# Optimization experiments

Measured on AMD Instinct MI355X. Metric: run time of the kernel, lower is better.

Reference implementation:

```python
import jax, jax.numpy as jnp
import numpy as np

HID = 1024; INTER = 2048; NSTATE = 16; KCONV = 4; DTRANK = 64
NHEADS = 16; NKV = 4; HDIM = 64; VHDIM = 128; EPS = 1e-6
ATTN_H = HID; K_H = NKV * HDIM; V_H = NKV * VHDIM
LATENT = INTER + ATTN_H + K_H + V_H  # 3840


def rmsnorm(x, w, eps=EPS):
    return x * jax.lax.rsqrt(jnp.mean(x * x, axis=-1, keepdims=True) + eps) * w


def setup_inputs():
    key = jax.random.key(0)
    ks = jax.random.split(key, 8)
    B, S = 2, 2048
    s = 0.02
    x = jax.random.normal(ks[0], (B, S, HID), jnp.float32)
    W_in = jax.random.normal(ks[1], (LATENT + INTER, HID), jnp.float32) * s
    conv_w = jax.random.normal(ks[2], (INTER, KCONV), jnp.float32) * 0.2
    conv_b = jnp.zeros((INTER,), jnp.float32)
    W_x = jax.random.normal(ks[3], (DTRANK + 2 * NSTATE, INTER), jnp.float32) * s
    dt_ln_w = jnp.ones((DTRANK,), jnp.float32)
    B_ln_w = jnp.ones((NSTATE,), jnp.float32)
    C_ln_w = jnp.ones((NSTATE,), jnp.float32)
    W_dt = jax.random.normal(ks[4], (INTER, DTRANK), jnp.float32) * s
    b_dt = jnp.log(jnp.expm1(jnp.full((INTER,), 0.01, jnp.float32)))
    A_log = jnp.log(jnp.broadcast_to(jnp.arange(1, NSTATE + 1, dtype=jnp.float32)[None, :], (INTER, NSTATE)))
    D_param = jnp.ones((INTER,), jnp.float32)
    ln1_w = jnp.ones((INTER,), jnp.float32)
    ln2_w = jnp.ones((INTER,), jnp.float32)
    W_out = jax.random.normal(ks[5], (HID, INTER), jnp.float32) * s
    return {"x": x, "W_in": W_in, "conv_w": conv_w, "conv_b": conv_b, "W_x": W_x,
            "dt_ln_w": dt_ln_w, "B_ln_w": B_ln_w, "C_ln_w": C_ln_w, "W_dt": W_dt,
            "b_dt": b_dt, "A_log": A_log, "D_param": D_param, "ln1_w": ln1_w,
            "ln2_w": ln2_w, "W_out": W_out}


def reference(x, W_in, conv_w, conv_b, W_x, dt_ln_w, B_ln_w, C_ln_w, W_dt, b_dt,
              A_log, D_param, ln1_w, ln2_w, W_out):
    Bsz, S, _ = x.shape
    proj = x @ W_in.T  # [B,S,LATENT+INTER]
    q = proj[..., :ATTN_H]
    k = proj[..., ATTN_H:ATTN_H + K_H]
    v = proj[..., ATTN_H + K_H:ATTN_H + K_H + V_H]
    xs = proj[..., ATTN_H + K_H + V_H:LATENT]
    gate = proj[..., LATENT:]

    # depthwise causal conv1d + silu (causal_conv1d_fn)
    xt = xs.transpose(0, 2, 1)  # [B,D,S]
    xc = jax.lax.conv_general_dilated(xt, conv_w[:, None, :], (1,), [(KCONV - 1, 0)],
                                      feature_group_count=INTER,
                                      dimension_numbers=("NCH", "OIH", "NCH"))
    xc = jax.nn.silu(xc + conv_b[None, :, None]).transpose(0, 2, 1)  # [B,S,D]

    # input-dependent dt, B, C with inner RMSNorms
    ssm_p = xc @ W_x.T  # [B,S,DTRANK+2N]
    dt = rmsnorm(ssm_p[..., :DTRANK], dt_ln_w)
    Bm = rmsnorm(ssm_p[..., DTRANK:DTRANK + NSTATE], B_ln_w)
    Cm = rmsnorm(ssm_p[..., DTRANK + NSTATE:], C_ln_w)
    delta = jax.nn.softplus(dt @ W_dt.T + b_dt)  # [B,S,D] (delta_bias + softplus)
    A = -jnp.exp(A_log)  # [D,N]

    def step(h, inp):
        d_t, b_t, c_t, x_t = inp  # [B,D],[B,N],[B,N],[B,D]
        dA = jnp.exp(d_t[:, :, None] * A)  # [B,D,N]
        h = h * dA + (d_t * x_t)[:, :, None] * b_t[:, None, :]
        y = jnp.einsum("bdn,bn->bd", h, c_t)
        return h, y

    h0 = jnp.zeros((Bsz, INTER, NSTATE), x.dtype)
    _, ys = jax.lax.scan(step, h0, (delta.transpose(1, 0, 2), Bm.transpose(1, 0, 2),
                                    Cm.transpose(1, 0, 2), xc.transpose(1, 0, 2)))
    y = ys.transpose(1, 0, 2) + xc * D_param
    y = y * jax.nn.silu(gate)  # gated scan output [B,S,INTER]

    # causal GQA attention branch (no output proj; v_head_dim = INTER/NHEADS)
    qh = q.reshape(Bsz, S, NHEADS, HDIM).transpose(0, 2, 1, 3)
    kh = jnp.repeat(k.reshape(Bsz, S, NKV, HDIM), NHEADS // NKV, axis=2).transpose(0, 2, 1, 3)
    vh = jnp.repeat(v.reshape(Bsz, S, NKV, VHDIM), NHEADS // NKV, axis=2).transpose(0, 2, 1, 3)
    scores = jnp.einsum("bhqd,bhkd->bhqk", qh, kh) * (1.0 / float(np.sqrt(HDIM)))
    mask = jnp.tril(jnp.ones((S, S), bool))
    scores = jnp.where(mask, scores, jnp.finfo(scores.dtype).min)
    attn = jnp.einsum("bhqk,bhkd->bhqd", jax.nn.softmax(scores, axis=-1), vh)
    attn = attn.transpose(0, 2, 1, 3).reshape(Bsz, S, INTER)

    out = (rmsnorm(attn, ln1_w) + rmsnorm(y, ln2_w)) * 0.5
    return out @ W_out.T
```

## Files before the change

### kernel.cpp

```cpp
#include <hip/hip_runtime.h>
#include <stdint.h>

#define HID    1024
#define INTER  2048
#define NSTATE 16
#define DTRANK 64
#define NHEADS 16
#define NKV    4
#define HDIM   64
#define VHDIM  128
#define ATTN_H 1024
#define K_H    256
#define V_H    512
#define LATENT 3840
#define NCOLS  5888
#define BATCH  2
#define SEQ    2048
#define T_TOT  4096
#define NCHUNK 64
#define CHLEN  32

typedef __bf16 bf16x8 __attribute__((ext_vector_type(8)));
typedef float  f32x4  __attribute__((ext_vector_type(4)));
typedef float  f32x4v __attribute__((ext_vector_type(4)));
typedef unsigned short u16x8 __attribute__((ext_vector_type(8)));

__device__ __forceinline__ float bf2f(unsigned short u) {
    return __uint_as_float(((unsigned int)u) << 16);
}
__device__ __forceinline__ unsigned short f2bf(float f) {
    unsigned int u = __float_as_uint(f);
    u = (u + 0x7fffu + ((u >> 16) & 1u)) >> 16;
    return (unsigned short)u;
}
__device__ __forceinline__ bf16x8 ldb8(const unsigned short* p) {
    return __builtin_bit_cast(bf16x8, *(const u16x8*)p);
}

typedef const __attribute__((address_space(1))) unsigned int* gas_ptr;
typedef __attribute__((address_space(3))) unsigned int* las_ptr;
__device__ __forceinline__ void load_lds16(const void* g, void* l) {
    __builtin_amdgcn_global_load_lds((gas_ptr)g, (las_ptr)l, 16, 0, 0);
}

__global__ void k_cvt(const float* __restrict__ src, unsigned short* __restrict__ dst, int n8) {
    int i = blockIdx.x * blockDim.x + threadIdx.x;
    if (i >= n8) return;
    f32x4v a = ((const f32x4v*)src)[2 * i];
    f32x4v b = ((const f32x4v*)src)[2 * i + 1];
    u16x8 o;
#pragma unroll
    for (int k = 0; k < 4; k++) { o[k] = f2bf(a[k]); o[k + 4] = f2bf(b[k]); }
    *(u16x8*)(dst + (size_t)i * 8) = o;
}

__global__ void k_wxpad(const float* __restrict__ W_x, unsigned short* __restrict__ Wxpad) {
    int i = blockIdx.x * blockDim.x + threadIdx.x;
    int e = i * 8;
    int row = e >> 11;
    int col = e & 2047;
    u16x8 o;
    if (row < DTRANK + 2 * NSTATE) {
#pragma unroll
        for (int k = 0; k < 8; k++) o[k] = f2bf(W_x[(size_t)row * INTER + col + k]);
    } else {
#pragma unroll
        for (int k = 0; k < 8; k++) o[k] = 0;
    }
    *(u16x8*)(Wxpad + e) = o;
}

template <int OUT_MODE>
__launch_bounds__(256)
__global__ void k_gemm(const unsigned short* __restrict__ A, const unsigned short* __restrict__ B,
                       void* __restrict__ Cout, const float* __restrict__ bias,
                       int M, int N, int K, int lda, int ldb, int ldc) {
    __shared__ __align__(16) unsigned short As[128 * 64];
    __shared__ __align__(16) unsigned short Bs[128 * 64];
    const int tid = threadIdx.x;
    const int lane = tid & 63;
    const int w = tid >> 6;
    const int wm = w >> 1, wn = w & 1;
    const int bm = blockIdx.y * 128, bn = blockIdx.x * 128;
    const size_t koff = (OUT_MODE == 3) ? (size_t)blockIdx.z * K : 0;

    f32x4 acc[4][4];
#pragma unroll
    for (int i = 0; i < 4; i++)
#pragma unroll
        for (int j = 0; j < 4; j++) acc[i][j] = (f32x4){0.f, 0.f, 0.f, 0.f};

    const int nk = K >> 6;
    for (int ks = 0; ks < nk; ++ks) {
        const int k0 = ks << 6;
#pragma unroll
        for (int i = 0; i < 4; ++i) {
            int qb = (w << 6) + (i << 8);
            int q = qb + lane;
            int row = q >> 3, c = q & 7;
            int csrc = c ^ (row & 7);
            load_lds16(A + (size_t)(bm + row) * lda + koff + k0 + csrc * 8, As + qb * 8);
            load_lds16(B + (size_t)(bn + row) * ldb + koff + k0 + csrc * 8, Bs + qb * 8);
        }
        __syncthreads();
#pragma unroll
        for (int kk = 0; kk < 2; ++kk) {
            bf16x8 af[4], bfr[4];
#pragma unroll
            for (int mi = 0; mi < 4; mi++) {
                int row = (wm << 6) + (mi << 4) + (lane & 15);
                int c = (kk << 2) + (lane >> 4);
                af[mi] = ldb8(As + row * 64 + (c ^ (row & 7)) * 8);
            }
#pragma unroll
            for (int ni = 0; ni < 4; ni++) {
                int row = (wn << 6) + (ni << 4) + (lane & 15);
                int c = (kk << 2) + (lane >> 4);
                bfr[ni] = ldb8(Bs + row * 64 + (c ^ (row & 7)) * 8);
            }
#pragma unroll
            for (int mi = 0; mi < 4; mi++)
#pragma unroll
                for (int ni = 0; ni < 4; ni++)
                    acc[mi][ni] = __builtin_amdgcn_mfma_f32_16x16x32_bf16(af[mi], bfr[ni], acc[mi][ni], 0, 0, 0);
        }
        __syncthreads();
    }
#pragma unroll
    for (int mi = 0; mi < 4; mi++)
#pragma unroll
        for (int ni = 0; ni < 4; ni++)
#pragma unroll
            for (int r = 0; r < 4; r++) {
                int grow = bm + (wm << 6) + (mi << 4) + ((lane >> 4) << 2) + r;
                int gcol = bn + (wn << 6) + (ni << 4) + (lane & 15);
                float v = acc[mi][ni][r];
                if (OUT_MODE == 0) {
                    ((unsigned short*)Cout)[(size_t)grow * ldc + gcol] = f2bf(v);
                } else if (OUT_MODE == 1) {
                    ((float*)Cout)[(size_t)grow * ldc + gcol] = v;
                } else if (OUT_MODE == 3) {
                    ((float*)Cout)[(size_t)blockIdx.z * M * ldc + (size_t)grow * ldc + gcol] = v;
                } else {
                    v += bias[gcol];
                    v = (v > 20.f) ? v : log1pf(__expf(v));
                    ((unsigned short*)Cout)[(size_t)grow * ldc + gcol] = f2bf(v);
                }
            }
}

__global__ void k_conv(const unsigned short* __restrict__ proj, const float* __restrict__ conv_w,
                       const float* __restrict__ conv_b, unsigned short* __restrict__ xc) {
    int r = blockIdx.x;
    int d8 = threadIdx.x * 8;
    int t = r & (SEQ - 1);
    float accv[8];
#pragma unroll
    for (int i = 0; i < 8; i++) accv[i] = conv_b[d8 + i];
#pragma unroll
    for (int j = 0; j < 4; j++) {
        int tp = t - 3 + j;
        if (tp < 0) continue;
        u16x8 xv = *(const u16x8*)(proj + (size_t)(r - 3 + j) * NCOLS + (LATENT - INTER) + d8);
#pragma unroll
        for (int i = 0; i < 8; i++) accv[i] += conv_w[(d8 + i) * 4 + j] * bf2f(xv[i]);
    }
    u16x8 o;
#pragma unroll
    for (int i = 0; i < 8; i++) {
        float v = accv[i];
        v = v / (1.f + __expf(-v));
        o[i] = f2bf(v);
    }
    *(u16x8*)(xc + (size_t)r * INTER + d8) = o;
}

__global__ void k_rms3(const float* __restrict__ ssmp, const float* __restrict__ dt_w,
                       const float* __restrict__ B_w, const float* __restrict__ C_w,
                       unsigned short* __restrict__ dtbf, float* __restrict__ Bm, float* __restrict__ Cm) {
    int r = blockIdx.x;
    int tid = threadIdx.x;
    int lane = tid & 63, w = tid >> 6;
    int c = tid;
    float v = 0.f;
    if (c < 96) {
#pragma unroll
        for (int s = 0; s < 8; s++) v += ssmp[(size_t)s * (T_TOT * 128) + (size_t)r * 128 + c];
    }
    float s = v * v;
    if (w == 0) {
#pragma unroll
        for (int d = 1; d < 64; d <<= 1) s += __shfl_xor(s, d);
        float rms = rsqrtf(s * (1.f / 64.f) + 1e-6f);
        dtbf[(size_t)r * 64 + lane] = f2bf(v * rms * dt_w[lane]);
    } else {
#pragma unroll
        for (int d = 1; d < 16; d <<= 1) s += __shfl_xor(s, d);
        float rms = rsqrtf(s * (1.f / 16.f) + 1e-6f);
        if (lane < 16) Bm[(size_t)r * 16 + lane] = v * rms * B_w[lane];
        else if (lane < 32) Cm[(size_t)r * 16 + (lane - 16)] = v * rms * C_w[lane - 16];
    }
}

template <int PASS>
__launch_bounds__(256)
__global__ void k_scan_chunk(const unsigned short* __restrict__ deltabf, const unsigned short* __restrict__ xcbf,
                             const float* __restrict__ Bm, const float* __restrict__ Cm,
                             const float* __restrict__ A_log,
                             float* __restrict__ hend, float* __restrict__ sumd,
                             const float* __restrict__ hinit, unsigned short* __restrict__ ybf) {
    __shared__ __align__(16) unsigned short dltS[CHLEN * 256];
    __shared__ __align__(16) unsigned short xvS[CHLEN * 256];
    __shared__ __align__(16) float BsT[CHLEN * 16];
    __shared__ __align__(16) float CsT[CHLEN * 16];
    const int d0 = blockIdx.x * 256;
    const int c = blockIdx.y;
    const int b = blockIdx.z;
    const int tid = threadIdx.x, lane = tid & 63, w = tid >> 6;
    const int t0 = c * CHLEN;
    const size_t rowbase = (size_t)(b * SEQ + t0);

    float An[16];
    {
        const f32x4* ap = (const f32x4*)(A_log + (size_t)(d0 + tid) * 16);
#pragma unroll
        for (int n4 = 0; n4 < 4; n4++) {
            f32x4 av = ap[n4];
#pragma unroll
            for (int j = 0; j < 4; j++) An[n4 * 4 + j] = -__expf(av[j]);
        }
    }

#pragma unroll
    for (int i = 0; i < 4; ++i) {
        int qb = (w << 6) + (i << 8);
        int q = qb + lane;
        int t = q >> 5, coff = q & 31;
        load_lds16(deltabf + (rowbase + t) * INTER + d0 + coff * 8, dltS + qb * 8);
        load_lds16(xcbf + (rowbase + t) * INTER + d0 + coff * 8, xvS + qb * 8);
    }
    if (tid < 128) {
        ((f32x4*)BsT)[tid] = ((const f32x4*)(Bm + rowbase * 16))[tid];
        if (PASS == 2) ((f32x4*)CsT)[tid] = ((const f32x4*)(Cm + rowbase * 16))[tid];
    }
    __syncthreads();

    const size_t sidx = ((size_t)(c * BATCH + b) * INTER + d0 + tid) * 16;
    float h[16];
    if (PASS == 2) {
        const f32x4* hp = (const f32x4*)(hinit + sidx);
#pragma unroll
        for (int n4 = 0; n4 < 4; n4++) {
            f32x4 hv = hp[n4];
#pragma unroll
            for (int j = 0; j < 4; j++) h[n4 * 4 + j] = hv[j];
        }
    } else {
#pragma unroll
        for (int n = 0; n < 16; n++) h[n] = 0.f;
    }
    float sd = 0.f;
    for (int t = 0; t < CHLEN; ++t) {
        float dlt = bf2f(dltS[t * 256 + tid]);
        float xv = bf2f(xvS[t * 256 + tid]);
        float dx = dlt * xv;
        if (PASS == 0) sd += dlt;
        float y = 0.f;
#pragma unroll
        for (int n4 = 0; n4 < 4; ++n4) {
            f32x4 Bt = ((f32x4*)BsT)[t * 4 + n4];
            f32x4 Ct;
            if (PASS == 2) Ct = ((f32x4*)CsT)[t * 4 + n4];
#pragma unroll
            for (int j = 0; j < 4; ++j) {
                int n = n4 * 4 + j;
                float a = __expf(dlt * An[n]);
                h[n] = h[n] * a + dx * Bt[j];
                if (PASS == 2) y += h[n] * Ct[j];
            }
        }
        if (PASS == 2) ybf[(rowbase + t) * INTER + d0 + tid] = f2bf(y);
    }
    if (PASS == 0) {
        f32x4* hp = (f32x4*)(hend + sidx);
#pragma unroll
        for (int n4 = 0; n4 < 4; n4++) {
            f32x4 hv;
#pragma unroll
            for (int j = 0; j < 4; j++) hv[j] = h[n4 * 4 + j];
            hp[n4] = hv;
        }
        sumd[(size_t)(c * BATCH + b) * INTER + d0 + tid] = sd;
    }
}

__global__ void k_scan_prop(const float* __restrict__ A_log, const float* __restrict__ hend,
                            const float* __restrict__ sumd, float* __restrict__ hinit) {
    const int tid = blockIdx.x * 256 + threadIdx.x;
    const int n = tid & 15;
    const int d = (tid >> 4) & (INTER - 1);
    const float An = -__expf(A_log[(size_t)d * 16 + n]);
    const int bd = tid >> 4;
    float h = 0.f;
#pragma unroll 1
    for (int cb = 0; cb < NCHUNK / 4; ++cb) {
        float he[4], sdv[4];
#pragma unroll
        for (int j = 0; j < 4; j++) {
            int c = cb * 4 + j;
            he[j] = hend[(size_t)c * 65536 + tid];
            sdv[j] = sumd[(size_t)c * 4096 + bd];
        }
#pragma unroll
        for (int j = 0; j < 4; j++) {
            int c = cb * 4 + j;
            hinit[(size_t)c * 65536 + tid] = h;
            h = he[j] + __expf(An * sdv[j]) * h;
        }
    }
}

__launch_bounds__(256)
__global__ void k_attn(const unsigned short* __restrict__ proj, unsigned short* __restrict__ attn) {
    __shared__ __align__(16) unsigned short Ks[64 * 64];
    __shared__ __align__(16) unsigned short Vt[128 * 64];
    __shared__ __align__(16) unsigned short Ps[4 * 16 * 64];
    const int pair = blockIdx.x;
    const int h = blockIdx.y;
    const int b = blockIdx.z;
    const int g = h >> 2;
    const int tid = threadIdx.x, lane = tid & 63, w = tid >> 6;
    const int l15 = lane & 15, hi = lane >> 4;

    const int krow = tid >> 3, kc = tid & 7;
    const int kp2 = (tid & 31) * 2, vb = tid >> 5;

    const unsigned short* kbase = proj + (size_t)(b * SEQ) * NCOLS + ATTN_H + g * HDIM;
    const unsigned short* vbase = proj + (size_t)(b * SEQ) * NCOLS + (ATTN_H + K_H) + g * VHDIM;

    u16x8 krA[2], vrA[2][2], krB[2], vrB[2][2];

    auto LOAD = [&](u16x8* kr, u16x8 (*vr)[2], int kv) {
        const unsigned short* kp_ = kbase + (size_t)(kv + krow) * NCOLS + kc * 8;
        kr[0] = *(const u16x8*)kp_;
        kr[1] = *(const u16x8*)(kp_ + (size_t)32 * NCOLS);
        const unsigned short* vp_ = vbase + (size_t)(kv + kp2) * NCOLS + vb * 8;
        vr[0][0] = *(const u16x8*)vp_;
        vr[0][1] = *(const u16x8*)(vp_ + NCOLS);
        vr[1][0] = *(const u16x8*)(vp_ + 64);
        vr[1][1] = *(const u16x8*)(vp_ + NCOLS + 64);
    };
    auto WRITE = [&](u16x8* kr, u16x8 (*vr)[2]) {
        int ksw = (kc ^ (krow & 7)) << 3;
        *(u16x8*)&Ks[krow * 64 + ksw] = kr[0];
        *(u16x8*)&Ks[(krow + 32) * 64 + ksw] = kr[1];
#pragma unroll
        for (int hf = 0; hf < 2; hf++) {
            u16x8 va = vr[hf][0], vb2 = vr[hf][1];
#pragma unroll
            for (int i = 0; i < 8; i++) {
                unsigned int pk = (unsigned int)va[i] | ((unsigned int)vb2[i] << 16);
                int r = (vb + hf * 8) * 8 + i;
                *(unsigned int*)&Vt[r * 64 + (((kp2 >> 3) ^ (r & 7)) << 3) + (kp2 & 7)] = pk;
            }
        }
    };

    const float SC = 0.18033688f;

    for (int phase = 0; phase < 2; ++phase) {
        const int qt = (phase == 0) ? (31 - pair) : pair;
        const int qw = qt * 64 + w * 16;
        const int ntiles = qt + 1;

        bf16x8 qf[2];
        {
            int qr = qw + l15;
            const unsigned short* qp = proj + (size_t)(b * SEQ + qr) * NCOLS + h * HDIM + hi * 8;
            qf[0] = ldb8(qp);
            qf[1] = ldb8(qp + 32);
        }
        f32x4 O[8];
#pragma unroll
        for (int vf = 0; vf < 8; vf++) O[vf] = (f32x4){0.f, 0.f, 0.f, 0.f};
        float l_[4] = {0.f, 0.f, 0.f, 0.f};

        auto COMPUTE = [&](int kv) {
            const int pbase = w * 1024;
            f32x4 sv[4];
#pragma unroll
            for (int cf = 0; cf < 4; ++cf) {
                f32x4 s = (f32x4){0.f, 0.f, 0.f, 0.f};
                int row = cf * 16 + l15;
#pragma unroll
                for (int kk = 0; kk < 2; ++kk) {
                    bf16x8 kb = ldb8(&Ks[row * 64 + ((((kk << 2) + hi) ^ (row & 7)) << 3)]);
                    s = __builtin_amdgcn_mfma_f32_16x16x32_bf16(qf[kk], kb, s, 0, 0, 0);
                }
                sv[cf] = s;
            }
            const int qi0 = qw + (hi << 2);
#pragma unroll
            for (int cf = 0; cf < 4; ++cf) {
                int ki = kv + cf * 16 + l15;
#pragma unroll
                for (int rg = 0; rg < 4; ++rg) {
                    float v = (ki <= qi0 + rg) ? exp2f(sv[cf][rg] * SC) : 0.f;
                    l_[rg] += v;
                    int pr = (hi << 2) + rg;
                    int pc = cf * 16 + l15;
                    Ps[pbase + pr * 64 + (((pc >> 3) ^ (pr & 7)) << 3) + (pc & 7)] = f2bf(v);
                }
            }
            bf16x8 pa0 = ldb8(&Ps[pbase + l15 * 64 + ((hi ^ (l15 & 7)) << 3)]);
            bf16x8 pa1 = ldb8(&Ps[pbase + l15 * 64 + (((4 + hi) ^ (l15 & 7)) << 3)]);
#pragma unroll
            for (int vf = 0; vf < 8; ++vf) {
                int vr_ = vf * 16 + l15;
                bf16x8 v0 = ldb8(&Vt[vr_ * 64 + ((hi ^ (vr_ & 7)) << 3)]);
                bf16x8 v1 = ldb8(&Vt[vr_ * 64 + (((4 + hi) ^ (vr_ & 7)) << 3)]);
                O[vf] = __builtin_amdgcn_mfma_f32_16x16x32_bf16(pa0, v0, O[vf], 0, 0, 0);
                O[vf] = __builtin_amdgcn_mfma_f32_16x16x32_bf16(pa1, v1, O[vf], 0, 0, 0);
            }
        };

        LOAD(krA, vrA, 0);
        bool useA = true;
        for (int j = 0; j < ntiles; ++j) {
            if (useA) {
                WRITE(krA, vrA);
                if (j + 1 < ntiles) LOAD(krB, vrB, (j + 1) * 64);
            } else {
                WRITE(krB, vrB);
                if (j + 1 < ntiles) LOAD(krA, vrA, (j + 1) * 64);
            }
            __syncthreads();
            COMPUTE(j * 64);
            __syncthreads();
            useA = !useA;
        }

#pragma unroll
        for (int dd = 1; dd < 16; dd <<= 1)
#pragma unroll
            for (int rg = 0; rg < 4; ++rg) l_[rg] += __shfl_xor(l_[rg], dd);
#pragma unroll
        for (int rg = 0; rg < 4; ++rg) {
            float inv = 1.f / l_[rg];
            int grow = b * SEQ + qw + (hi << 2) + rg;
#pragma unroll
            for (int vf = 0; vf < 8; ++vf) {
                int gcol = h * VHDIM + vf * 16 + l15;
                attn[(size_t)grow * INTER + gcol] = f2bf(O[vf][rg] * inv);
            }
        }
    }
}

__launch_bounds__(256)
__global__ void k_fuse(const unsigned short* __restrict__ attn, const unsigned short* __restrict__ ybf,
                       const unsigned short* __restrict__ xc, const unsigned short* __restrict__ proj,
                       const float* __restrict__ Dp, const float* __restrict__ ln1,
                       const float* __restrict__ ln2, unsigned short* __restrict__ fused) {
    __shared__ float red[8];
    int r = blockIdx.x, tid = threadIdx.x;
    int c8 = tid * 8;
    u16x8 av = *(const u16x8*)(attn + (size_t)r * INTER + c8);
    u16x8 yv8 = *(const u16x8*)(ybf + (size_t)r * INTER + c8);
    u16x8 xv8 = *(const u16x8*)(xc + (size_t)r * INTER + c8);
    u16x8 gv8 = *(const u16x8*)(proj + (size_t)r * NCOLS + LATENT + c8);
    float a_[8], y_[8];
    float ssa = 0.f, ssy = 0.f;
#pragma unroll
    for (int i = 0; i < 8; i++) {
        float a = bf2f(av[i]);
        float yv = bf2f(yv8[i]) + bf2f(xv8[i]) * Dp[c8 + i];
        float gg = bf2f(gv8[i]);
        yv *= gg / (1.f + __expf(-gg));
        a_[i] = a; y_[i] = yv;
        ssa += a * a; ssy += yv * yv;
    }
#pragma unroll
    for (int d = 1; d < 64; d <<= 1) { ssa += __shfl_xor(ssa, d); ssy += __shfl_xor(ssy, d); }
    int w = tid >> 6, lane = tid & 63;
    if (lane == 0) { red[w * 2] = ssa; red[w * 2 + 1] = ssy; }
    __syncthreads();
    ssa = red[0] + red[2] + red[4] + red[6];
    ssy = red[1] + red[3] + red[5] + red[7];
    float ra = rsqrtf(ssa * (1.f / 2048.f) + 1e-6f);
    float ry = rsqrtf(ssy * (1.f / 2048.f) + 1e-6f);
    u16x8 o;
#pragma unroll
    for (int i = 0; i < 8; i++) {
        float v = (a_[i] * ra * ln1[c8 + i] + y_[i] * ry * ln2[c8 + i]) * 0.5f;
        o[i] = f2bf(v);
    }
    *(u16x8*)(fused + (size_t)r * INTER + c8) = o;
}

extern "C" void kernel_launch(void* const* d_in, const int* in_sizes, int n_in,
                              void* d_out, int out_size, void* d_ws, size_t ws_size,
                              hipStream_t stream) {
    const float* x      = (const float*)d_in[0];
    const float* W_in   = (const float*)d_in[1];
    const float* conv_w = (const float*)d_in[2];
    const float* conv_b = (const float*)d_in[3];
    const float* W_x    = (const float*)d_in[4];
    const float* dt_w   = (const float*)d_in[5];
    const float* B_w    = (const float*)d_in[6];
    const float* C_w    = (const float*)d_in[7];
    const float* W_dt   = (const float*)d_in[8];
    const float* b_dt   = (const float*)d_in[9];
    const float* A_log  = (const float*)d_in[10];
    const float* Dp     = (const float*)d_in[11];
    const float* ln1    = (const float*)d_in[12];
    const float* ln2    = (const float*)d_in[13];
    const float* W_out  = (const float*)d_in[14];
    float* out = (float*)d_out;

    char* p = (char*)d_ws;
    auto alloc = [&](size_t bytes) -> void* {
        void* r = (void*)p;
        p += (bytes + 255) & ~(size_t)255;
        return r;
    };
    unsigned short* xbf     = (unsigned short*)alloc((size_t)T_TOT * HID * 2);
    unsigned short* Winbf   = (unsigned short*)alloc((size_t)NCOLS * HID * 2);
    unsigned short* projbf  = (unsigned short*)alloc((size_t)T_TOT * NCOLS * 2);
    unsigned short* xcbf    = (unsigned short*)alloc((size_t)T_TOT * INTER * 2);
    unsigned short* Wxpad   = (unsigned short*)alloc((size_t)128 * INTER * 2);
    float*          ssmp    = (float*)alloc((size_t)8 * T_TOT * 128 * 4);
    unsigned short* dtbf    = (unsigned short*)alloc((size_t)T_TOT * DTRANK * 2);
    float*          Bm      = (float*)alloc((size_t)T_TOT * 16 * 4);
    float*          Cm      = (float*)alloc((size_t)T_TOT * 16 * 4);
    unsigned short* Wdtbf   = (unsigned short*)alloc((size_t)INTER * DTRANK * 2);
    unsigned short* deltabf = (unsigned short*)alloc((size_t)T_TOT * INTER * 2);
    unsigned short* ybf     = (unsigned short*)alloc((size_t)T_TOT * INTER * 2);
    unsigned short* attnbf  = (unsigned short*)alloc((size_t)T_TOT * INTER * 2);
    unsigned short* fusedbf = (unsigned short*)alloc((size_t)T_TOT * INTER * 2);
    unsigned short* Woutbf  = (unsigned short*)alloc((size_t)HID * INTER * 2);
    float*          hendws  = (float*)alloc((size_t)NCHUNK * BATCH * INTER * 16 * 4);
    float*          hinitws = (float*)alloc((size_t)NCHUNK * BATCH * INTER * 16 * 4);
    float*          sumdws  = (float*)alloc((size_t)NCHUNK * BATCH * INTER * 4);

    k_cvt<<<(T_TOT * HID / 8 + 255) / 256, 256, 0, stream>>>(x, xbf, T_TOT * HID / 8);
    k_cvt<<<(NCOLS * HID / 8 + 255) / 256, 256, 0, stream>>>(W_in, Winbf, NCOLS * HID / 8);
    k_cvt<<<(INTER * DTRANK / 8 + 255) / 256, 256, 0, stream>>>(W_dt, Wdtbf, INTER * DTRANK / 8);
    k_cvt<<<(HID * INTER / 8 + 255) / 256, 256, 0, stream>>>(W_out, Woutbf, HID * INTER / 8);
    k_wxpad<<<(128 * INTER / 8) / 256, 256, 0, stream>>>(W_x, Wxpad);

    k_gemm<0><<<dim3(NCOLS / 128, T_TOT / 128), 256, 0, stream>>>(
        xbf, Winbf, projbf, nullptr, T_TOT, NCOLS, HID, HID, HID, NCOLS);
    k_conv<<<T_TOT, 256, 0, stream>>>(projbf, conv_w, conv_b, xcbf);
    k_gemm<3><<<dim3(1, T_TOT / 128, 8), 256, 0, stream>>>(
        xcbf, Wxpad, ssmp, nullptr, T_TOT, 128, 256, INTER, INTER, 128);
    k_rms3<<<T_TOT, 128, 0, stream>>>(ssmp, dt_w, B_w, C_w, dtbf, Bm, Cm);
    k_gemm<2><<<dim3(INTER / 128, T_TOT / 128), 256, 0, stream>>>(
        dtbf, Wdtbf, deltabf, b_dt, T_TOT, INTER, DTRANK, DTRANK, DTRANK, INTER);
    k_scan_chunk<0><<<dim3(INTER / 256, NCHUNK, BATCH), 256, 0, stream>>>(
        deltabf, xcbf, Bm, Cm, A_log, hendws, sumdws, nullptr, nullptr);
    k_scan_prop<<<256, 256, 0, stream>>>(A_log, hendws, sumdws, hinitws);
    k_scan_chunk<2><<<dim3(INTER / 256, NCHUNK, BATCH), 256, 0, stream>>>(
        deltabf, xcbf, Bm, Cm, A_log, nullptr, nullptr, hinitws, ybf);
    k_attn<<<dim3(16, NHEADS, BATCH), 256, 0, stream>>>(projbf, attnbf);
    k_fuse<<<T_TOT, 256, 0, stream>>>(attnbf, ybf, xcbf, projbf, Dp, ln1, ln2, fusedbf);
    k_gemm<1><<<dim3(HID / 128, T_TOT / 128), 256, 0, stream>>>(
        fusedbf, Woutbf, out, nullptr, T_TOT, HID, INTER, INTER, INTER, HID);
}
```

Before: 406.7 us.

## Merge prep conversions, use exp2 in scan, split attention blocks, skip mask

Folds the four fp32-to-bf16 conversion launches and the W_x padding launch into one prep kernel, which removes launch overhead. The scan kernels fold log2(e) into A so they can call exp2f directly. The attention kernel no longer pairs a long and a short query tile in one block; it launches one block per query tile, heaviest first, which gives 1024 blocks instead of 512. The causal mask is now applied only on the diagonal KV tile. Finer blocks improve load balance, at the cost of more blocks and reloading Q per block.

Result: slower. 488.8 us (+20.2%).

```diff
diff --git a/kernel.cpp b/kernel.cpp
--- a/kernel.cpp
+++ b/kernel.cpp
@@ -19,6 +19,7 @@
 #define T_TOT  4096
 #define NCHUNK 64
 #define CHLEN  32
+#define LOG2E  1.44269504f
 
 typedef __bf16 bf16x8 __attribute__((ext_vector_type(8)));
 typedef float  f32x4  __attribute__((ext_vector_type(4)));
@@ -43,31 +44,38 @@
     __builtin_amdgcn_global_load_lds((gas_ptr)g, (las_ptr)l, 16, 0, 0);
 }
 
-__global__ void k_cvt(const float* __restrict__ src, unsigned short* __restrict__ dst, int n8) {
-    int i = blockIdx.x * blockDim.x + threadIdx.x;
-    if (i >= n8) return;
-    f32x4v a = ((const f32x4v*)src)[2 * i];
-    f32x4v b = ((const f32x4v*)src)[2 * i + 1];
+__global__ void k_prep(const float* __restrict__ x, const float* __restrict__ W_in,
+                       const float* __restrict__ W_dt, const float* __restrict__ W_out,
+                       const float* __restrict__ W_x,
+                       unsigned short* __restrict__ xbf, unsigned short* __restrict__ Winbf,
+                       unsigned short* __restrict__ Wdtbf, unsigned short* __restrict__ Woutbf,
+                       unsigned short* __restrict__ Wxpad) {
+    int i = blockIdx.x * 256 + threadIdx.x;
+    const float* src; unsigned short* dst; int off;
+    if (i < 524288)        { src = x;     dst = xbf;    off = i; }
+    else if (i < 1277952)  { src = W_in;  dst = Winbf;  off = i - 524288; }
+    else if (i < 1294336)  { src = W_dt;  dst = Wdtbf;  off = i - 1277952; }
+    else if (i < 1556480)  { src = W_out; dst = Woutbf; off = i - 1294336; }
+    else {
+        int e = (i - 1556480) * 8;
+        int row = e >> 11, col = e & 2047;
+        u16x8 o;
+        if (row < DTRANK + 2 * NSTATE) {
+#pragma unroll
+            for (int k = 0; k < 8; k++) o[k] = f2bf(W_x[(size_t)row * INTER + col + k]);
+        } else {
+#pragma unroll
+            for (int k = 0; k < 8; k++) o[k] = 0;
+        }
+        *(u16x8*)(Wxpad + e) = o;
+        return;
+    }
+    f32x4v a = ((const f32x4v*)src)[2 * off];
+    f32x4v b = ((const f32x4v*)src)[2 * off + 1];
     u16x8 o;
 #pragma unroll
     for (int k = 0; k < 4; k++) { o[k] = f2bf(a[k]); o[k + 4] = f2bf(b[k]); }
-    *(u16x8*)(dst + (size_t)i * 8) = o;
-}
-
-__global__ void k_wxpad(const float* __restrict__ W_x, unsigned short* __restrict__ Wxpad) {
-    int i = blockIdx.x * blockDim.x + threadIdx.x;
-    int e = i * 8;
-    int row = e >> 11;
-    int col = e & 2047;
-    u16x8 o;
-    if (row < DTRANK + 2 * NSTATE) {
-#pragma unroll
-        for (int k = 0; k < 8; k++) o[k] = f2bf(W_x[(size_t)row * INTER + col + k]);
-    } else {
-#pragma unroll
-        for (int k = 0; k < 8; k++) o[k] = 0;
-    }
-    *(u16x8*)(Wxpad + e) = o;
+    *(u16x8*)(dst + (size_t)off * 8) = o;
 }
 
 template <int OUT_MODE>
@@ -227,7 +235,7 @@
         for (int n4 = 0; n4 < 4; n4++) {
             f32x4 av = ap[n4];
 #pragma unroll
-            for (int j = 0; j < 4; j++) An[n4 * 4 + j] = -__expf(av[j]);
+            for (int j = 0; j < 4; j++) An[n4 * 4 + j] = -LOG2E * __expf(av[j]);
         }
     }
 
@@ -274,7 +282,7 @@
 #pragma unroll
             for (int j = 0; j < 4; ++j) {
                 int n = n4 * 4 + j;
-                float a = __expf(dlt * An[n]);
+                float a = exp2f(dlt * An[n]);
                 h[n] = h[n] * a + dx * Bt[j];
                 if (PASS == 2) y += h[n] * Ct[j];
             }
@@ -299,7 +307,7 @@
     const int tid = blockIdx.x * 256 + threadIdx.x;
     const int n = tid & 15;
     const int d = (tid >> 4) & (INTER - 1);
-    const float An = -__expf(A_log[(size_t)d * 16 + n]);
+    const float An = -LOG2E * __expf(A_log[(size_t)d * 16 + n]);
     const int bd = tid >> 4;
     float h = 0.f;
 #pragma unroll 1
@@ -315,7 +323,7 @@
         for (int j = 0; j < 4; j++) {
             int c = cb * 4 + j;
             hinit[(size_t)c * 65536 + tid] = h;
-            h = he[j] + __expf(An * sdv[j]) * h;
+            h = he[j] + exp2f(An * sdv[j]) * h;
         }
     }
 }
@@ -325,7 +333,7 @@
     __shared__ __align__(16) unsigned short Ks[64 * 64];
     __shared__ __align__(16) unsigned short Vt[128 * 64];
     __shared__ __align__(16) unsigned short Ps[4 * 16 * 64];
-    const int pair = blockIdx.x;
+    const int qt = (gridDim.x - 1) - blockIdx.x;
     const int h = blockIdx.y;
     const int b = blockIdx.z;
     const int g = h >> 2;
@@ -367,92 +375,91 @@
     };
 
     const float SC = 0.18033688f;
-
-    for (int phase = 0; phase < 2; ++phase) {
-        const int qt = (phase == 0) ? (31 - pair) : pair;
-        const int qw = qt * 64 + w * 16;
-        const int ntiles = qt + 1;
-
-        bf16x8 qf[2];
-        {
-            int qr = qw + l15;
-            const unsigned short* qp = proj + (size_t)(b * SEQ + qr) * NCOLS + h * HDIM + hi * 8;
-            qf[0] = ldb8(qp);
-            qf[1] = ldb8(qp + 32);
-        }
-        f32x4 O[8];
-#pragma unroll
-        for (int vf = 0; vf < 8; vf++) O[vf] = (f32x4){0.f, 0.f, 0.f, 0.f};
-        float l_[4] = {0.f, 0.f, 0.f, 0.f};
-
-        auto COMPUTE = [&](int kv) {
-            const int pbase = w * 1024;
-            f32x4 sv[4];
-#pragma unroll
-            for (int cf = 0; cf < 4; ++cf) {
-                f32x4 s = (f32x4){0.f, 0.f, 0.f, 0.f};
-                int row = cf * 16 + l15;
-#pragma unroll
-                for (int kk = 0; kk < 2; ++kk) {
-                    bf16x8 kb = ldb8(&Ks[row * 64 + ((((kk << 2) + hi) ^ (row & 7)) << 3)]);
-                    s = __builtin_amdgcn_mfma_f32_16x16x32_bf16(qf[kk], kb, s, 0, 0, 0);
-                }
-                sv[cf] = s;
-            }
-            const int qi0 = qw + (hi << 2);
-#pragma unroll
-            for (int cf = 0; cf < 4; ++cf) {
-                int ki = kv + cf * 16 + l15;
-#pragma unroll
-                for (int rg = 0; rg < 4; ++rg) {
-                    float v = (ki <= qi0 + rg) ? exp2f(sv[cf][rg] * SC) : 0.f;
-                    l_[rg] += v;
-                    int pr = (hi << 2) + rg;
-                    int pc = cf * 16 + l15;
-                    Ps[pbase + pr * 64 + (((pc >> 3) ^ (pr & 7)) << 3) + (pc & 7)] = f2bf(v);
-                }
-            }
-            bf16x8 pa0 = ldb8(&Ps[pbase + l15 * 64 + ((hi ^ (l15 & 7)) << 3)]);
-            bf16x8 pa1 = ldb8(&Ps[pbase + l15 * 64 + (((4 + hi) ^ (l15 & 7)) << 3)]);
-#pragma unroll
-            for (int vf = 0; vf < 8; ++vf) {
-                int vr_ = vf * 16 + l15;
-                bf16x8 v0 = ldb8(&Vt[vr_ * 64 + ((hi ^ (vr_ & 7)) << 3)]);
-                bf16x8 v1 = ldb8(&Vt[vr_ * 64 + (((4 + hi) ^ (vr_ & 7)) << 3)]);
-                O[vf] = __builtin_amdgcn_mfma_f32_16x16x32_bf16(pa0, v0, O[vf], 0, 0, 0);
-                O[vf] = __builtin_amdgcn_mfma_f32_16x16x32_bf16(pa1, v1, O[vf], 0, 0, 0);
-            }
-        };
-
-        LOAD(krA, vrA, 0);
-        bool useA = true;
-        for (int j = 0; j < ntiles; ++j) {
-            if (useA) {
-                WRITE(krA, vrA);
-                if (j + 1 < ntiles) LOAD(krB, vrB, (j + 1) * 64);
-            } else {
-                WRITE(krB, vrB);
-                if (j + 1 < ntiles) LOAD(krA, vrA, (j + 1) * 64);
-            }
-            __syncthreads();
-            COMPUTE(j * 64);
-            __syncthreads();
-            useA = !useA;
-        }
-
-#pragma unroll
-        for (int dd = 1; dd < 16; dd <<= 1)
-#pragma unroll
-            for (int rg = 0; rg < 4; ++rg) l_[rg] += __shfl_xor(l_[rg], dd);
-#pragma unroll
-        for (int rg = 0; rg < 4; ++rg) {
-            float inv = 1.f / l_[rg];
-            int grow = b * SEQ + qw + (hi << 2) + rg;
-#pragma unroll
-            for (int vf = 0; vf < 8; ++vf) {
-                int gcol = h * VHDIM + vf * 16 + l15;
-                attn[(size_t)grow * INTER + gcol] = f2bf(O[vf][rg] * inv);
-            }
+    const int qw = qt * 64 + w * 16;
+    const int ntiles = qt + 1;
+
+    bf16x8 qf[2];
+    {
+        int qr = qw + l15;
+        const unsigned short* qp = proj + (size_t)(b * SEQ + qr) * NCOLS + h * HDIM + hi * 8;
+        qf[0] = ldb8(qp);
+        qf[1] = ldb8(qp + 32);
+    }
+    f32x4 O[8];
+#pragma unroll
+    for (int vf = 0; vf < 8; vf++) O[vf] = (f32x4){0.f, 0.f, 0.f, 0.f};
+    float l_[4] = {0.f, 0.f, 0.f, 0.f};
+
+    auto COMPUTE = [&](int kv, bool MASK) {
+        const int pbase = w * 1024;
+        f32x4 sv[4];
+#pragma unroll
+        for (int cf = 0; cf < 4; ++cf) {
+            f32x4 s = (f32x4){0.f, 0.f, 0.f, 0.f};
+            int row = cf * 16 + l15;
+#pragma unroll
+            for (int kk = 0; kk < 2; ++kk) {
+                bf16x8 kb = ldb8(&Ks[row * 64 + ((((kk << 2) + hi) ^ (row & 7)) << 3)]);
+                s = __builtin_amdgcn_mfma_f32_16x16x32_bf16(qf[kk], kb, s, 0, 0, 0);
+            }
+            sv[cf] = s;
+        }
+        const int qi0 = qw + (hi << 2);
+#pragma unroll
+        for (int cf = 0; cf < 4; ++cf) {
+            int ki = kv + cf * 16 + l15;
+#pragma unroll
+            for (int rg = 0; rg < 4; ++rg) {
+                float v;
+                if (MASK) v = (ki <= qi0 + rg) ? exp2f(sv[cf][rg] * SC) : 0.f;
+                else      v = exp2f(sv[cf][rg] * SC);
+                l_[rg] += v;
+                int pr = (hi << 2) + rg;
+                int pc = cf * 16 + l15;
+                Ps[pbase + pr * 64 + (((pc >> 3) ^ (pr & 7)) << 3) + (pc & 7)] = f2bf(v);
+            }
+        }
+        bf16x8 pa0 = ldb8(&Ps[pbase + l15 * 64 + ((hi ^ (l15 & 7)) << 3)]);
+        bf16x8 pa1 = ldb8(&Ps[pbase + l15 * 64 + (((4 + hi) ^ (l15 & 7)) << 3)]);
+#pragma unroll
+        for (int vf = 0; vf < 8; ++vf) {
+            int vr_ = vf * 16 + l15;
+            bf16x8 v0 = ldb8(&Vt[vr_ * 64 + ((hi ^ (vr_ & 7)) << 3)]);
+            bf16x8 v1 = ldb8(&Vt[vr_ * 64 + (((4 + hi) ^ (vr_ & 7)) << 3)]);
+            O[vf] = __builtin_amdgcn_mfma_f32_16x16x32_bf16(pa0, v0, O[vf], 0, 0, 0);
+            O[vf] = __builtin_amdgcn_mfma_f32_16x16x32_bf16(pa1, v1, O[vf], 0, 0, 0);
+        }
+    };
+
+    LOAD(krA, vrA, 0);
+    bool useA = true;
+    for (int j = 0; j < ntiles; ++j) {
+        if (useA) {
+            WRITE(krA, vrA);
+            if (j + 1 < ntiles) LOAD(krB, vrB, (j + 1) * 64);
+        } else {
+            WRITE(krB, vrB);
+            if (j + 1 < ntiles) LOAD(krA, vrA, (j + 1) * 64);
+        }
+        __syncthreads();
+        if (j == ntiles - 1) COMPUTE(j * 64, true);
+        else                 COMPUTE(j * 64, false);
+        __syncthreads();
+        useA = !useA;
+    }
+
+#pragma unroll
+    for (int dd = 1; dd < 16; dd <<= 1)
+#pragma unroll
+        for (int rg = 0; rg < 4; ++rg) l_[rg] += __shfl_xor(l_[rg], dd);
+#pragma unroll
+    for (int rg = 0; rg < 4; ++rg) {
+        float inv = 1.f / l_[rg];
+        int grow = b * SEQ + qw + (hi << 2) + rg;
+#pragma unroll
+        for (int vf = 0; vf < 8; ++vf) {
+            int gcol = h * VHDIM + vf * 16 + l15;
+            attn[(size_t)grow * INTER + gcol] = f2bf(O[vf][rg] * inv);
         }
     }
 }
@@ -543,11 +550,7 @@
     float*          hinitws = (float*)alloc((size_t)NCHUNK * BATCH * INTER * 16 * 4);
     float*          sumdws  = (float*)alloc((size_t)NCHUNK * BATCH * INTER * 4);
 
-    k_cvt<<<(T_TOT * HID / 8 + 255) / 256, 256, 0, stream>>>(x, xbf, T_TOT * HID / 8);
-    k_cvt<<<(NCOLS * HID / 8 + 255) / 256, 256, 0, stream>>>(W_in, Winbf, NCOLS * HID / 8);
-    k_cvt<<<(INTER * DTRANK / 8 + 255) / 256, 256, 0, stream>>>(W_dt, Wdtbf, INTER * DTRANK / 8);
-    k_cvt<<<(HID * INTER / 8 + 255) / 256, 256, 0, stream>>>(W_out, Woutbf, HID * INTER / 8);
-    k_wxpad<<<(128 * INTER / 8) / 256, 256, 0, stream>>>(W_x, Wxpad);
+    k_prep<<<6208, 256, 0, stream>>>(x, W_in, W_dt, W_out, W_x, xbf, Winbf, Wdtbf, Woutbf, Wxpad);
 
     k_gemm<0><<<dim3(NCOLS / 128, T_TOT / 128), 256, 0, stream>>>(
         xbf, Winbf, projbf, nullptr, T_TOT, NCOLS, HID, HID, HID, NCOLS);
@@ -562,7 +565,7 @@
     k_scan_prop<<<256, 256, 0, stream>>>(A_log, hendws, sumdws, hinitws);
     k_scan_chunk<2><<<dim3(INTER / 256, NCHUNK, BATCH), 256, 0, stream>>>(
         deltabf, xcbf, Bm, Cm, A_log, nullptr, nullptr, hinitws, ybf);
-    k_attn<<<dim3(16, NHEADS, BATCH), 256, 0, stream>>>(projbf, attnbf);
+    k_attn<<<dim3(32, NHEADS, BATCH), 256, 0, stream>>>(projbf, attnbf);
     k_fuse<<<T_TOT, 256, 0, stream>>>(attnbf, ybf, xcbf, projbf, Dp, ln1, ln2, fusedbf);
     k_gemm<1><<<dim3(HID / 128, T_TOT / 128), 256, 0, stream>>>(
         fusedbf, Woutbf, out, nullptr, T_TOT, HID, INTER, INTER, INTER, HID);
```
